# Performance work log

Hardware: AMD Instinct MI355X
Metric: run time of the kernel (lower is better)

## Reference

```python
import jax, jax.numpy as jnp
import numpy as np

B, N, H, D = 1, 4096, 16, 64
C = H * D  # 1024
SCALE = D ** -0.5


def setup_inputs() -> dict:
    key = jax.random.key(0)
    k1, k2, k3, k4 = jax.random.split(key, 4)
    x = jax.random.normal(k1, (B, N, C), dtype=jnp.float32)
    # torch nn.Linear weights: [out_features, in_features]; y = x @ W.T + b
    w_qkv = jax.random.normal(k2, (3 * C, C), dtype=jnp.float32) * 0.02
    w_proj = jax.random.normal(k3, (C, C), dtype=jnp.float32) * 0.02
    b_proj = jax.random.normal(k4, (C,), dtype=jnp.float32) * 0.02
    return {"x": x, "w_qkv": w_qkv, "w_proj": w_proj, "b_proj": b_proj}


def reference(x, w_qkv, w_proj, b_proj):
    Bn, Nn, Cn = x.shape
    # fused QKV projection (no bias)
    qkv = jnp.einsum('bnc,oc->bno', x, w_qkv)            # [B,N,3C]
    qkv = qkv.reshape(Bn, Nn, 3, H, D)
    q = jnp.transpose(qkv[:, :, 0], (0, 2, 1, 3))        # [B,H,N,D]
    k = jnp.transpose(qkv[:, :, 1], (0, 2, 1, 3))
    v = jnp.transpose(qkv[:, :, 2], (0, 2, 1, 3))
    attn = jnp.einsum('bhnd,bhmd->bhnm', q, k) * SCALE   # [B,H,N,N]
    causal_mask = jnp.triu(jnp.ones((Nn, Nn), dtype=bool), k=1)
    attn = jnp.where(causal_mask, -jnp.inf, attn)
    attn = jax.nn.softmax(attn, axis=-1)
    out = jnp.einsum('bhnm,bhmd->bhnd', attn, v)          # [B,H,N,D]
    out = jnp.transpose(out, (0, 2, 1, 3)).reshape(Bn, Nn, Cn)
    out = jnp.einsum('bnc,oc->bno', out, w_proj) + b_proj
    return out
```

## Files before the change

kernel.cpp:

```cpp
#include <hip/hip_runtime.h>
#include <hip/hip_bf16.h>
#include <stdint.h>
#include <stddef.h>

using bf16 = __hip_bfloat16;
typedef short short8 __attribute__((ext_vector_type(8)));
typedef short short4v __attribute__((ext_vector_type(4)));
typedef short short2v __attribute__((ext_vector_type(2)));
typedef float f32x4 __attribute__((ext_vector_type(4)));

#define MFMA16(A, B, C) __builtin_amdgcn_mfma_f32_16x16x32_bf16(A, B, C, 0, 0, 0)
#define MFMA16K16(A, B, C) __builtin_amdgcn_mfma_f32_16x16x16bf16_1k(A, B, C, 0, 0, 0)
#define GLOAD_LDS(g, l) __builtin_amdgcn_global_load_lds( \
    (const __attribute__((address_space(1))) void*)(g),   \
    (__attribute__((address_space(3))) void*)(l), 16, 0, 0)

constexpr int AN  = 4096;
constexpr int NH  = 16;
constexpr int HD  = 64;
constexpr int CC  = 1024;
constexpr int C3  = 3072;
constexpr float QSCALE = 0.125f * 1.4426950408889634f;

__device__ inline short bf16s(float f) {
    bf16 h = __float2bfloat16(f);
    return *reinterpret_cast<short*>(&h);
}
__device__ inline float bf2f(short s) {
    return __uint_as_float(((unsigned)(unsigned short)s) << 16);
}
__device__ inline short4v pack4(float a, float b, float c, float d) {
    union { short4v s4; __hip_bfloat162 h2[2]; } u;
    u.h2[0] = __float22bfloat162_rn(make_float2(a, b));
    u.h2[1] = __float22bfloat162_rn(make_float2(c, d));
    return u.s4;
}

__global__ void detect_mode(const unsigned short* __restrict__ xraw,
                            int* __restrict__ mode) {
    const int lane = threadIdx.x;
    int crazy = 0;
    #pragma unroll
    for (int i = 0; i < 4; ++i) {
        const unsigned short u = xraw[lane * 4 + i];
        const int e = (u >> 7) & 0xFF;
        if (e >= 134 || (e != 0 && e <= 110)) ++crazy;
    }
    #pragma unroll
    for (int off = 32; off > 0; off >>= 1)
        crazy += __shfl_down(crazy, off, 64);
    if (lane == 0) *mode = (crazy >= 8) ? 1 : 0;
}

__device__ inline void cast8(const void* __restrict__ src,
                             bf16* __restrict__ dst, int i, int m) {
    if (m) {
        const float* s = (const float*)src;
        float4 a = *(const float4*)(s + i);
        float4 b = *(const float4*)(s + i + 4);
        short8 o;
        o[0] = bf16s(a.x); o[1] = bf16s(a.y); o[2] = bf16s(a.z); o[3] = bf16s(a.w);
        o[4] = bf16s(b.x); o[5] = bf16s(b.y); o[6] = bf16s(b.z); o[7] = bf16s(b.w);
        *(short8*)(dst + i) = o;
    } else {
        *(short8*)(dst + i) = *(const short8*)((const short*)src + i);
    }
}

__global__ void cast_all(const void* __restrict__ x, const void* __restrict__ wq,
                         const void* __restrict__ wp, const void* __restrict__ bp,
                         bf16* __restrict__ xb, bf16* __restrict__ wqb,
                         bf16* __restrict__ wpb, float* __restrict__ biasf,
                         const int* __restrict__ mode) {
    const int b = blockIdx.x;
    const int tid = threadIdx.x;
    const int m = *mode;
    if (b < 2048) {
        cast8(x, xb, (b * 256 + tid) * 8, m);
    } else if (b < 3584) {
        cast8(wq, wqb, ((b - 2048) * 256 + tid) * 8, m);
    } else if (b < 4096) {
        cast8(wp, wpb, ((b - 3584) * 256 + tid) * 8, m);
    } else {
        #pragma unroll
        for (int i = tid; i < CC; i += 256)
            biasf[i] = m ? ((const float*)bp)[i] : bf2f(((const short*)bp)[i]);
    }
}

constexpr int BM = 128, BN = 128, BK = 32;

__global__ __launch_bounds__(256, 3) void gemm_qkv(
    const bf16* __restrict__ A, const bf16* __restrict__ Bw,
    bf16* __restrict__ Cout, bf16* __restrict__ vTout)
{
    __shared__ bf16 As[BM * BK];
    __shared__ bf16 Bs[BN * BK];

    const int tid  = threadIdx.x;
    const int wave = tid >> 6;
    const int lane = tid & 63;
    const int quad = lane >> 4;
    const int l16  = lane & 15;
    const int wr   = wave >> 1;
    const int wc   = wave & 1;
    const int m0   = blockIdx.y * BM;
    const int o0   = blockIdx.x * BN;

    const int srow = lane >> 2;
    const int scol = (lane & 3) * 8;

    f32x4 acc[4][4] = {};

    for (int k0 = 0; k0 < CC; k0 += BK) {
        __syncthreads();
        #pragma unroll
        for (int c = 0; c < 2; ++c) {
            const int rbase = wave * 32 + c * 16;
            GLOAD_LDS(A + (size_t)(m0 + rbase + srow) * CC + k0 + scol, &As[rbase * BK]);
            GLOAD_LDS(Bw + (size_t)(o0 + rbase + srow) * CC + k0 + scol, &Bs[rbase * BK]);
        }
        __syncthreads();

        short8 af[4], bfr[4];
        #pragma unroll
        for (int i = 0; i < 4; ++i)
            af[i] = *(const short8*)&As[(wr * 64 + i * 16 + l16) * BK + quad * 8];
        #pragma unroll
        for (int j = 0; j < 4; ++j)
            bfr[j] = *(const short8*)&Bs[(wc * 64 + j * 16 + l16) * BK + quad * 8];
        #pragma unroll
        for (int i = 0; i < 4; ++i)
            #pragma unroll
            for (int j = 0; j < 4; ++j)
                acc[i][j] = MFMA16(af[i], bfr[j], acc[i][j]);
    }

    if (o0 >= 2 * CC) {
        #pragma unroll
        for (int j = 0; j < 4; ++j) {
            const int vc = o0 - 2 * CC + wc * 64 + j * 16 + l16;
            #pragma unroll
            for (int i = 0; i < 4; ++i) {
                const int row0 = m0 + wr * 64 + i * 16 + quad * 4;
                *(short4v*)&vTout[(size_t)vc * AN + row0] =
                    pack4(acc[i][j][0], acc[i][j][1], acc[i][j][2], acc[i][j][3]);
            }
        }
        return;
    }
    const float qs = (o0 < CC) ? QSCALE : 1.0f;
    #pragma unroll
    for (int j = 0; j < 4; ++j) {
        const int col = o0 + wc * 64 + j * 16 + l16;
        #pragma unroll
        for (int i = 0; i < 4; ++i) {
            const int row = m0 + wr * 64 + i * 16 + quad * 4;
            #pragma unroll
            for (int r = 0; r < 4; ++r)
                Cout[(size_t)(row + r) * C3 + col] = __float2bfloat16(acc[i][j][r] * qs);
        }
    }
}

constexpr int PM = 128, PN = 64, PK = 32;

__global__ __launch_bounds__(256, 2) void gemm_proj(
    const bf16* __restrict__ A, const bf16* __restrict__ Bw,
    const float* __restrict__ bias, void* __restrict__ Cout,
    const int* __restrict__ mode)
{
    __shared__ bf16 As[PM * PK];
    __shared__ bf16 Bs[PN * PK];

    const int tid  = threadIdx.x;
    const int wave = tid >> 6;
    const int lane = tid & 63;
    const int quad = lane >> 4;
    const int l16  = lane & 15;
    const int wr   = wave >> 1;
    const int wc   = wave & 1;
    const int m0   = blockIdx.y * PM;
    const int o0   = blockIdx.x * PN;
    const bool f32out = (*mode != 0);

    const int srow = lane >> 2;
    const int scol = (lane & 3) * 8;

    f32x4 acc[4][2] = {};

    for (int k0 = 0; k0 < CC; k0 += PK) {
        __syncthreads();
        #pragma unroll
        for (int c = 0; c < 2; ++c) {
            const int rbase = wave * 32 + c * 16;
            GLOAD_LDS(A + (size_t)(m0 + rbase + srow) * CC + k0 + scol, &As[rbase * PK]);
        }
        {
            const int rbase = wave * 16;
            GLOAD_LDS(Bw + (size_t)(o0 + rbase + srow) * CC + k0 + scol, &Bs[rbase * PK]);
        }
        __syncthreads();

        short8 af[4], bfr[2];
        #pragma unroll
        for (int i = 0; i < 4; ++i)
            af[i] = *(const short8*)&As[(wr * 64 + i * 16 + l16) * PK + quad * 8];
        #pragma unroll
        for (int j = 0; j < 2; ++j)
            bfr[j] = *(const short8*)&Bs[(wc * 32 + j * 16 + l16) * PK + quad * 8];
        #pragma unroll
        for (int i = 0; i < 4; ++i)
            #pragma unroll
            for (int j = 0; j < 2; ++j)
                acc[i][j] = MFMA16(af[i], bfr[j], acc[i][j]);
    }

    #pragma unroll
    for (int j = 0; j < 2; ++j) {
        const int col = o0 + wc * 32 + j * 16 + l16;
        const float bv = bias[col];
        #pragma unroll
        for (int i = 0; i < 4; ++i) {
            const int row = m0 + wr * 64 + i * 16 + quad * 4;
            #pragma unroll
            for (int r = 0; r < 4; ++r) {
                const float v = acc[i][j][r] + bv;
                const size_t idx = (size_t)(row + r) * CC + col;
                if (f32out) ((float*)Cout)[idx] = v;
                else        ((bf16*)Cout)[idx]  = __float2bfloat16(v);
            }
        }
    }
}

constexpr int TK = 64;

__global__ __launch_bounds__(256, 4) void attn5(
    const bf16* __restrict__ qkv, const bf16* __restrict__ vT,
    bf16* __restrict__ pOn, float* __restrict__ pl)
{
    __shared__ bf16 Ks[2][TK * HD];
    __shared__ bf16 Vs[2][HD * TK];

    const int tid  = threadIdx.x;
    const int wave = tid >> 6;
    const int lane = tid & 63;
    const int quad = lane >> 4;
    const int l16  = lane & 15;
    const int h7   = l16 & 7;
    const int h    = blockIdx.x & 15;
    const int t    = blockIdx.x >> 4;

    short4v ones;
    ones[0] = (short)0x3F80; ones[1] = (short)0x3F80;
    ones[2] = (short)0x3F80; ones[3] = (short)0x3F80;

    const int sr = lane >> 3;
    const int pc = lane & 7;

    #pragma unroll 1
    for (int pp = 0; pp < 2; ++pp) {
        const int tile = pp ? 63 - t : t;
        const int nIt  = tile + 1;
        const int i0   = pp ? ((64 - t) + 1) >> 1 : 0;
        const int i1   = pp ? 64 - t : (t + 2) >> 1;
        const int half = pp;
        const int qw   = tile * 64 + wave * 16;

        short8 qf0, qf1;
        {
            const bf16* qp = qkv + (size_t)(qw + l16) * C3 + h * HD + quad * 8;
            qf0 = *(const short8*)qp;
            qf1 = *(const short8*)(qp + 32);
        }

        f32x4 acc_l = {};
        f32x4 acc_o[4] = {};

        if (i0 < i1) {
            const bf16 *kp[2], *vp[2];
            #pragma unroll
            for (int c = 0; c < 2; ++c) {
                const int row = wave * 16 + c * 8 + sr;
                const int lc  = pc ^ (row & 7);
                kp[c] = qkv + (size_t)(i0 * TK + row) * C3 + CC + h * HD + lc * 8;
                vp[c] = vT + (size_t)(h * HD + row) * AN + i0 * TK + lc * 8;
            }
            auto stage = [&](int p) {
                #pragma unroll
                for (int c = 0; c < 2; ++c) {
                    const int rb = wave * 16 + c * 8;
                    GLOAD_LDS(kp[c], &Ks[p][rb * HD]);
                    GLOAD_LDS(vp[c], &Vs[p][rb * TK]);
                    kp[c] += (size_t)TK * C3;
                    vp[c] += TK;
                }
            };
            stage(0);
            __syncthreads();
            const bool hasdiag = (i1 == nIt);

            for (int it = i0; it < i1; ++it) {
                const int p = (it - i0) & 1;
                if (it + 1 < i1) stage(p ^ 1);

                f32x4 st[4];
                #pragma unroll
                for (int tt = 0; tt < 4; ++tt) {
                    const int row = tt * 16 + l16;
                    short8 kf0 = *(const short8*)&Ks[p][row * HD + ((quad ^ h7) * 8)];
                    short8 kf1 = *(const short8*)&Ks[p][row * HD + (((quad + 4) ^ h7) * 8)];
                    f32x4 a = {};
                    a = MFMA16(kf0, qf0, a);
                    a = MFMA16(kf1, qf1, a);
                    st[tt] = a;
                }

                if (hasdiag && it == i1 - 1) {
                    const int q = qw + l16;
                    const int kv0 = it * TK;
                    #pragma unroll
                    for (int tt = 0; tt < 4; ++tt)
                        #pragma unroll
                        for (int r = 0; r < 4; ++r) {
                            const int kv = kv0 + tt * 16 + quad * 4 + r;
                            st[tt][r] = (kv <= q) ? exp2f(st[tt][r]) : 0.0f;
                        }
                } else {
                    #pragma unroll
                    for (int tt = 0; tt < 4; ++tt)
                        #pragma unroll
                        for (int r = 0; r < 4; ++r)
                            st[tt][r] = exp2f(st[tt][r]);
                }

                #pragma unroll
                for (int tt = 0; tt < 4; ++tt) {
                    const short4v bp = pack4(st[tt][0], st[tt][1], st[tt][2], st[tt][3]);
                    acc_l = MFMA16K16(ones, bp, acc_l);
                    const int pc2 = (2 * tt + (quad >> 1)) ^ h7;
                    #pragma unroll
                    for (int dt = 0; dt < 4; ++dt) {
                        const int row = dt * 16 + l16;
                        short4v vf = *(const short4v*)&Vs[p][row * TK + pc2 * 8 + (quad & 1) * 4];
                        acc_o[dt] = MFMA16K16(vf, bp, acc_o[dt]);
                    }
                }
                __syncthreads();
            }
        }

        const size_t base = (size_t)half * AN * CC + (size_t)(qw + l16) * CC + h * HD;
        #pragma unroll
        for (int dt = 0; dt < 4; ++dt) {
            const int d0 = dt * 16 + quad * 4;
            *(short4v*)&pOn[base + d0] =
                pack4(acc_o[dt][0], acc_o[dt][1], acc_o[dt][2], acc_o[dt][3]);
        }
        if (quad == 0)
            pl[(size_t)half * NH * AN + (size_t)h * AN + qw + l16] = acc_l[0];
    }
}

__global__ __launch_bounds__(128) void combine_halves(
    const bf16* __restrict__ pOn, const float* __restrict__ pl,
    bf16* __restrict__ outp)
{
    const int q  = blockIdx.x;
    const int c0 = threadIdx.x * 8;
    const int h  = c0 >> 6;
    const float l0 = pl[(size_t)h * AN + q];
    const float l1 = pl[(size_t)NH * AN + (size_t)h * AN + q];
    const float L = l0 + l1;
    const float invL = (L > 0.f) ? 1.f / L : 0.f;
    const size_t off = (size_t)q * CC + c0;
    short8 o0 = *(const short8*)&pOn[off];
    short8 o1 = *(const short8*)&pOn[(size_t)AN * CC + off];
    short8 o;
    #pragma unroll
    for (int e = 0; e < 8; e += 2) {
        float v0 = (bf2f(o0[e])     + bf2f(o1[e]))     * invL;
        float v1 = (bf2f(o0[e + 1]) + bf2f(o1[e + 1])) * invL;
        union { short2v s2; __hip_bfloat162 h2; } u;
        u.h2 = __float22bfloat162_rn(make_float2(v0, v1));
        o[e] = u.s2[0]; o[e + 1] = u.s2[1];
    }
    *(short8*)&outp[off] = o;
}

extern "C" void kernel_launch(void* const* d_in, const int* in_sizes, int n_in,
                              void* d_out, int out_size, void* d_ws, size_t ws_size,
                              hipStream_t stream) {
    char* ws = (char*)d_ws;
    bf16*   qkv      = (bf16*)(ws);
    bf16*   attn_out = (bf16*)(ws + 25165824);
    bf16*   vT       = (bf16*)(ws + 33554432);
    bf16*   xb       = (bf16*)(ws + 41943040);
    bf16*   wqkvb    = (bf16*)(ws + 50331648);
    bf16*   wprojb   = (bf16*)(ws + 56623104);
    float*  biasf    = (float*)(ws + 58720256);
    int*    mode     = (int*)(ws + 58724352);
    bf16*   pOn      = (bf16*)(ws + 58728448);
    float*  pl       = (float*)(ws + 75505664);

    detect_mode<<<1, 64, 0, stream>>>((const unsigned short*)d_in[0], mode);
    cast_all<<<dim3(4097), 256, 0, stream>>>(
        d_in[0], d_in[1], d_in[2], d_in[3], xb, wqkvb, wprojb, biasf, mode);

    gemm_qkv<<<dim3(C3 / BN, AN / BM), 256, 0, stream>>>(xb, wqkvb, qkv, vT);
    attn5<<<dim3(64 * NH), 256, 0, stream>>>(qkv, vT, pOn, pl);
    combine_halves<<<dim3(AN), 128, 0, stream>>>(pOn, pl, attn_out);
    gemm_proj<<<dim3(CC / PN, AN / PM), 256, 0, stream>>>(
        attn_out, wprojb, biasf, d_out, mode);
}
```

Baseline: 212.2 us.

## Inline dtype detection into cast kernel and use hardware bf16 pack and fast exp2

Removes the separate single-block detect_mode launch by having every block of cast_all recompute the dtype check from the first 256 input elements, with one block still writing the mode flag for the projection GEMM. Replaces the library bf16 conversions with a packed hardware convert builtin (or a round-half-up fallback) in casts and epilogues, and swaps exp2f for the amdgcn fast exp2 builtin in the attention softmax. The intent is to save one kernel launch plus conversion and exp instruction overhead. In exchange every cast block re-reads the sample, and the fallback rounding and fast exp2 differ slightly from the prior numerics.

```diff
diff --git a/kernel.cpp b/kernel.cpp
--- a/kernel.cpp
+++ b/kernel.cpp
@@ -23,22 +23,43 @@
 constexpr float QSCALE = 0.125f * 1.4426950408889634f;
 
 __device__ inline short bf16s(float f) {
-    bf16 h = __float2bfloat16(f);
-    return *reinterpret_cast<short*>(&h);
+    return (short)((__float_as_uint(f) + 0x8000u) >> 16);
 }
 __device__ inline float bf2f(short s) {
     return __uint_as_float(((unsigned)(unsigned short)s) << 16);
 }
+__device__ inline bf16 sbf(short s) {
+    union { short s; bf16 b; } u;
+    u.s = s;
+    return u.b;
+}
+#if __has_builtin(__builtin_amdgcn_cvt_pk_bf16_f32)
+typedef __bf16 bf16x2 __attribute__((ext_vector_type(2)));
+__device__ inline short2v pk2(float a, float b) {
+    bf16x2 r = __builtin_amdgcn_cvt_pk_bf16_f32(a, b);
+    return *(short2v*)&r;
+}
+#else
+__device__ inline short2v pk2(float a, float b) {
+    unsigned ua = __float_as_uint(a) + 0x8000u;
+    unsigned ub = __float_as_uint(b) + 0x8000u;
+    unsigned r  = __builtin_amdgcn_perm(ub, ua, 0x07060302);
+    return *(short2v*)&r;
+}
+#endif
 __device__ inline short4v pack4(float a, float b, float c, float d) {
-    union { short4v s4; __hip_bfloat162 h2[2]; } u;
-    u.h2[0] = __float22bfloat162_rn(make_float2(a, b));
-    u.h2[1] = __float22bfloat162_rn(make_float2(c, d));
-    return u.s4;
-}
-
-__global__ void detect_mode(const unsigned short* __restrict__ xraw,
-                            int* __restrict__ mode) {
-    const int lane = threadIdx.x;
+    short2v lo = pk2(a, b), hi = pk2(c, d);
+    short4v r;
+    r[0] = lo[0]; r[1] = lo[1]; r[2] = hi[0]; r[3] = hi[1];
+    return r;
+}
+#if __has_builtin(__builtin_amdgcn_exp2f)
+#define FAST_EXP2(x) __builtin_amdgcn_exp2f(x)
+#else
+#define FAST_EXP2(x) exp2f(x)
+#endif
+
+__device__ inline int detect_mode_inline(const unsigned short* xraw, int lane) {
     int crazy = 0;
     #pragma unroll
     for (int i = 0; i < 4; ++i) {
@@ -49,7 +70,8 @@
     #pragma unroll
     for (int off = 32; off > 0; off >>= 1)
         crazy += __shfl_down(crazy, off, 64);
-    if (lane == 0) *mode = (crazy >= 8) ? 1 : 0;
+    crazy = __shfl(crazy, 0, 64);
+    return (crazy >= 8) ? 1 : 0;
 }
 
 __device__ inline void cast8(const void* __restrict__ src,
@@ -59,8 +81,10 @@
         float4 a = *(const float4*)(s + i);
         float4 b = *(const float4*)(s + i + 4);
         short8 o;
-        o[0] = bf16s(a.x); o[1] = bf16s(a.y); o[2] = bf16s(a.z); o[3] = bf16s(a.w);
-        o[4] = bf16s(b.x); o[5] = bf16s(b.y); o[6] = bf16s(b.z); o[7] = bf16s(b.w);
+        short2v p0 = pk2(a.x, a.y), p1 = pk2(a.z, a.w);
+        short2v p2 = pk2(b.x, b.y), p3 = pk2(b.z, b.w);
+        o[0] = p0[0]; o[1] = p0[1]; o[2] = p1[0]; o[3] = p1[1];
+        o[4] = p2[0]; o[5] = p2[1]; o[6] = p3[0]; o[7] = p3[1];
         *(short8*)(dst + i) = o;
     } else {
         *(short8*)(dst + i) = *(const short8*)((const short*)src + i);
@@ -71,10 +95,10 @@
                          const void* __restrict__ wp, const void* __restrict__ bp,
                          bf16* __restrict__ xb, bf16* __restrict__ wqb,
                          bf16* __restrict__ wpb, float* __restrict__ biasf,
-                         const int* __restrict__ mode) {
+                         int* __restrict__ mode) {
     const int b = blockIdx.x;
     const int tid = threadIdx.x;
-    const int m = *mode;
+    const int m = detect_mode_inline((const unsigned short*)x, tid & 63);
     if (b < 2048) {
         cast8(x, xb, (b * 256 + tid) * 8, m);
     } else if (b < 3584) {
@@ -85,6 +109,7 @@
         #pragma unroll
         for (int i = tid; i < CC; i += 256)
             biasf[i] = m ? ((const float*)bp)[i] : bf2f(((const short*)bp)[i]);
+        if (tid == 0) *mode = m;
     }
 }
 
@@ -157,8 +182,11 @@
         for (int i = 0; i < 4; ++i) {
             const int row = m0 + wr * 64 + i * 16 + quad * 4;
             #pragma unroll
-            for (int r = 0; r < 4; ++r)
-                Cout[(size_t)(row + r) * C3 + col] = __float2bfloat16(acc[i][j][r] * qs);
+            for (int r = 0; r < 2; ++r) {
+                short2v p = pk2(acc[i][j][2 * r] * qs, acc[i][j][2 * r + 1] * qs);
+                Cout[(size_t)(row + 2 * r) * C3 + col]     = sbf(p[0]);
+                Cout[(size_t)(row + 2 * r + 1) * C3 + col] = sbf(p[1]);
+            }
         }
     }
 }
@@ -223,12 +251,17 @@
         #pragma unroll
         for (int i = 0; i < 4; ++i) {
             const int row = m0 + wr * 64 + i * 16 + quad * 4;
-            #pragma unroll
-            for (int r = 0; r < 4; ++r) {
-                const float v = acc[i][j][r] + bv;
-                const size_t idx = (size_t)(row + r) * CC + col;
-                if (f32out) ((float*)Cout)[idx] = v;
-                else        ((bf16*)Cout)[idx]  = __float2bfloat16(v);
+            if (f32out) {
+                #pragma unroll
+                for (int r = 0; r < 4; ++r)
+                    ((float*)Cout)[(size_t)(row + r) * CC + col] = acc[i][j][r] + bv;
+            } else {
+                #pragma unroll
+                for (int r = 0; r < 2; ++r) {
+                    short2v p = pk2(acc[i][j][2 * r] + bv, acc[i][j][2 * r + 1] + bv);
+                    ((bf16*)Cout)[(size_t)(row + 2 * r) * CC + col]     = sbf(p[0]);
+                    ((bf16*)Cout)[(size_t)(row + 2 * r + 1) * CC + col] = sbf(p[1]);
+                }
             }
         }
     }
@@ -325,14 +358,14 @@
                         #pragma unroll
                         for (int r = 0; r < 4; ++r) {
                             const int kv = kv0 + tt * 16 + quad * 4 + r;
-                            st[tt][r] = (kv <= q) ? exp2f(st[tt][r]) : 0.0f;
+                            st[tt][r] = (kv <= q) ? FAST_EXP2(st[tt][r]) : 0.0f;
                         }
                 } else {
                     #pragma unroll
                     for (int tt = 0; tt < 4; ++tt)
                         #pragma unroll
                         for (int r = 0; r < 4; ++r)
-                            st[tt][r] = exp2f(st[tt][r]);
+                            st[tt][r] = FAST_EXP2(st[tt][r]);
                 }
 
                 #pragma unroll
@@ -382,9 +415,8 @@
     for (int e = 0; e < 8; e += 2) {
         float v0 = (bf2f(o0[e])     + bf2f(o1[e]))     * invL;
         float v1 = (bf2f(o0[e + 1]) + bf2f(o1[e + 1])) * invL;
-        union { short2v s2; __hip_bfloat162 h2; } u;
-        u.h2 = __float22bfloat162_rn(make_float2(v0, v1));
-        o[e] = u.s2[0]; o[e + 1] = u.s2[1];
+        short2v p = pk2(v0, v1);
+        o[e] = p[0]; o[e + 1] = p[1];
     }
     *(short8*)&outp[off] = o;
 }
@@ -404,7 +436,6 @@
     bf16*   pOn      = (bf16*)(ws + 58728448);
     float*  pl       = (float*)(ws + 75505664);
 
-    detect_mode<<<1, 64, 0, stream>>>((const unsigned short*)d_in[0], mode);
     cast_all<<<dim3(4097), 256, 0, stream>>>(
         d_in[0], d_in[1], d_in[2], d_in[3], xb, wqkvb, wprojb, biasf, mode);
 
```

After: 201.6 us. -5.0%, faster.
